# Performance work log

Hardware: AMD Instinct MI355X
Metric: run time of the kernel (lower is better)

## Reference

```python
import jax, jax.numpy as jnp
import numpy as np

OUTPUT_DIM = 1024
D_K = 1024  # Lt feature dim
D_Q = 1024  # rnn_ht feature dim
SCALE = 1.0 / np.sqrt(64.0)  # hardcoded 64**0.5 in original, NOT sqrt(output_dim)


def setup_inputs() -> dict:
    key = jax.random.key(0)
    k1, k2, k3, k4 = jax.random.split(key, 4)
    B, Sq, Sk = 8, 2048, 2048
    Lt = jax.random.normal(k1, (B, Sk, D_K), dtype=jnp.float32)
    rnn_ht = jax.random.normal(k2, (B, Sq, D_Q), dtype=jnp.float32)
    # 'uniform' keras initializer: U(-0.05, 0.05)
    kernel = jax.random.uniform(k3, (2, D_K, OUTPUT_DIM), dtype=jnp.float32, minval=-0.05, maxval=0.05)
    W = jax.random.uniform(k4, (D_Q, OUTPUT_DIM), dtype=jnp.float32, minval=-0.05, maxval=0.05)
    return {"Lt": Lt, "rnn_ht": rnn_ht, "kernel": kernel, "W": W}


def reference(Lt, rnn_ht, kernel, W):
    WQ = jnp.einsum('bsd,de->bse', rnn_ht, W)          # [B, Sq, E]
    WK = jnp.einsum('bsd,de->bse', Lt, kernel[0])      # [B, Sk, E]
    WV = jnp.einsum('bsd,de->bse', Lt, kernel[1])      # [B, Sk, E]
    QK = jnp.einsum('bqe,bke->bqk', WQ, WK) * SCALE    # [B, Sq, Sk]
    weights = jax.nn.softmax(QK, axis=-1)
    context_vector = jnp.einsum('bqk,bke->bqe', weights, WV)  # [B, Sq, E]
    return (context_vector, weights)
```

## Files before the change

### kernel.cpp

```cpp
#include <hip/hip_runtime.h>


typedef __bf16 bf16x8 __attribute__((ext_vector_type(8)));
typedef __bf16 bf16x4 __attribute__((ext_vector_type(4)));
typedef float  f32x4  __attribute__((ext_vector_type(4)));

__device__ __forceinline__ void gload_lds16(const void* g, void* l) {
  __builtin_amdgcn_global_load_lds(
      (__attribute__((address_space(1))) void*)(g),
      (__attribute__((address_space(3))) void*)(uintptr_t)(l),
      16, 0, 0);
}

__device__ __forceinline__ void ldfrag4(bf16x8 (&f)[4], const __bf16* reg_,
                                        int rbase, int fm, int gq) {
#pragma unroll
  for (int i = 0; i < 4; ++i) {
    const int r = rbase + i * 16 + fm;
    f[i] = *(const bf16x8*)(reg_ + r * 32 + ((gq ^ ((r >> 1) & 3)) << 3));
  }
}

__device__ __forceinline__ void stage16(const __bf16* src, __bf16* dst,
                                        size_t rowstride, int wave, int lane) {
#pragma unroll
  for (int i = 0; i < 2; ++i) {
    const int chunk = wave * 2 + i;
    const int row = chunk * 16 + (lane >> 2);
    const int gg = (lane & 3) ^ ((row >> 1) & 3);
    gload_lds16(src + (size_t)row * rowstride + (gg << 3), dst + chunk * 512);
  }
}

template <int MH>
__device__ __forceinline__ void mfma16(f32x4 (&acc)[8][4], const bf16x8 (&a)[4],
                                       const bf16x8 (&b)[4]) {
#pragma unroll
  for (int mi = 0; mi < 4; ++mi)
#pragma unroll
    for (int nj = 0; nj < 4; ++nj)
      acc[MH * 4 + mi][nj] = __builtin_amdgcn_mfma_f32_16x16x32_bf16(
          a[mi], b[nj], acc[MH * 4 + mi][nj], 0, 0, 0);
}

#define PHASE_MID()                       \
  __builtin_amdgcn_sched_barrier(0);      \
  __builtin_amdgcn_s_barrier();           \
  __builtin_amdgcn_s_setprio(1)

#define PHASE_END()                       \
  __builtin_amdgcn_s_setprio(0);          \
  __builtin_amdgcn_sched_barrier(0);      \
  __builtin_amdgcn_s_barrier()

template <bool OUTBF16>
__device__ __forceinline__ void tile_gemm(
    const __bf16* __restrict__ Aa, const __bf16* __restrict__ Ba,
    void* __restrict__ Cp, size_t cbase, int N, int K, float scale,
    __bf16* lds, int wave, int lane, int wm, int wn, int fm, int gq) {
  __bf16* const As_ = lds;
  __bf16* const Bs_ = lds + 32768;
#define AREG(p, h) (As_ + (p) * 16384 + (h) * 8192)
#define BREG(p, h) (Bs_ + (p) * 16384 + (h) * 8192)

  f32x4 acc[8][4] = {};
  bf16x8 a[4], b[4];

  stage16(Ba + 0,  BREG(0, 0), K, wave, lane);
  stage16(Aa + 0,  AREG(0, 0), K, wave, lane);
  stage16(Ba + 32, BREG(0, 1), K, wave, lane);
  stage16(Aa + 32, AREG(0, 1), K, wave, lane);
  asm volatile("s_waitcnt vmcnt(4)" ::: "memory");
  stage16(Ba + 64, BREG(1, 0), K, wave, lane);
  stage16(Aa + 64, AREG(1, 0), K, wave, lane);
  stage16(Ba + 96, BREG(1, 1), K, wave, lane);
  asm volatile("s_waitcnt vmcnt(6)" ::: "memory");
  __builtin_amdgcn_s_barrier();

  const int niter = K >> 7;
  for (int it = 0; it < niter; ++it) {
    const int kt = it << 7;
    const bool s2 = (kt + 128) < K;

    ldfrag4(a, AREG(0, 0), wm, fm, gq);
    ldfrag4(b, BREG(0, 0), wn, fm, gq);
    stage16(Aa + kt + 96, AREG(1, 1), K, wave, lane);
    PHASE_MID();
    mfma16<0>(acc, a, b);
    PHASE_END();

    ldfrag4(a, AREG(0, 0), wm + 64, fm, gq);
    if (s2) stage16(Ba + kt + 128, BREG(0, 0), K, wave, lane);
    PHASE_MID();
    mfma16<1>(acc, a, b);
    PHASE_END();

    ldfrag4(a, AREG(0, 1), wm, fm, gq);
    ldfrag4(b, BREG(0, 1), wn, fm, gq);
    if (s2) stage16(Aa + kt + 128, AREG(0, 0), K, wave, lane);
    PHASE_MID();
    mfma16<0>(acc, a, b);
    PHASE_END();

    ldfrag4(a, AREG(0, 1), wm + 64, fm, gq);
    if (s2) stage16(Ba + kt + 160, BREG(0, 1), K, wave, lane);
    PHASE_MID();
    mfma16<1>(acc, a, b);
    __builtin_amdgcn_s_setprio(0);
    __builtin_amdgcn_sched_barrier(0);
    if (s2) { asm volatile("s_waitcnt vmcnt(6)" ::: "memory"); }
    else    { asm volatile("s_waitcnt vmcnt(0)" ::: "memory"); }
    __builtin_amdgcn_s_barrier();

    ldfrag4(a, AREG(1, 0), wm, fm, gq);
    ldfrag4(b, BREG(1, 0), wn, fm, gq);
    if (s2) stage16(Aa + kt + 160, AREG(0, 1), K, wave, lane);
    PHASE_MID();
    mfma16<0>(acc, a, b);
    PHASE_END();

    ldfrag4(a, AREG(1, 0), wm + 64, fm, gq);
    if (s2) stage16(Ba + kt + 192, BREG(1, 0), K, wave, lane);
    PHASE_MID();
    mfma16<1>(acc, a, b);
    PHASE_END();

    ldfrag4(a, AREG(1, 1), wm, fm, gq);
    ldfrag4(b, BREG(1, 1), wn, fm, gq);
    if (s2) stage16(Aa + kt + 192, AREG(1, 0), K, wave, lane);
    PHASE_MID();
    mfma16<0>(acc, a, b);
    PHASE_END();

    ldfrag4(a, AREG(1, 1), wm + 64, fm, gq);
    if (s2) stage16(Ba + kt + 224, BREG(1, 1), K, wave, lane);
    PHASE_MID();
    mfma16<1>(acc, a, b);
    __builtin_amdgcn_s_setprio(0);
    __builtin_amdgcn_sched_barrier(0);
    if (s2) { asm volatile("s_waitcnt vmcnt(6)" ::: "memory"); }
    __builtin_amdgcn_s_barrier();
  }

  const int col   = lane & 15;
  const int rquad = (lane >> 4) * 4;
#pragma unroll
  for (int mi = 0; mi < 8; ++mi) {
#pragma unroll
    for (int r = 0; r < 4; ++r) {
      const size_t roff = (size_t)(wm + mi * 16 + rquad + r) * (size_t)N;
#pragma unroll
      for (int nj = 0; nj < 4; ++nj) {
        const size_t cidx = cbase + roff + wn + nj * 16 + col;
        if constexpr (OUTBF16) {
          ((__bf16*)Cp)[cidx] = (__bf16)acc[mi][nj][r];
        } else {
          ((float*)Cp)[cidx] = acc[mi][nj][r] * scale;
        }
      }
    }
  }
#undef AREG
#undef BREG
}

__global__ __launch_bounds__(512, 2)
void proj_all(const __bf16* __restrict__ rnnb, const __bf16* __restrict__ Ltb,
              const __bf16* __restrict__ Wt, const __bf16* __restrict__ k0t,
              const __bf16* __restrict__ k1t, __bf16* __restrict__ WQ,
              __bf16* __restrict__ WK, __bf16* __restrict__ WVt) {
  __shared__ __bf16 lds[65536];
  const int tid = threadIdx.x, wave = tid >> 6, lane = tid & 63;
  const int wm = (wave >> 2) * 128, wn = (wave & 3) * 64;
  const int fm = lane & 15, gq = lane >> 4;
  const int d = blockIdx.x, x = d & 7, s = d >> 3;

  {
    const int bx = s & 3, by = x * 8 + (s >> 2);
    const size_t ao = (size_t)by * 256 * 1024;
    const size_t bo = (size_t)bx * 256 * 1024;
    const size_t cb = (size_t)by * 256 * 1024 + (size_t)bx * 256;
    tile_gemm<true>(rnnb + ao, Wt + bo, WQ, cb, 1024, 1024, 1.0f,
                    lds, wave, lane, wm, wn, fm, gq);
    tile_gemm<true>(Ltb + ao, k0t + bo, WK, cb, 1024, 1024, 1.0f,
                    lds, wave, lane, wm, wn, fm, gq);
  }
  {
    const int by = s >> 3, bx = s & 7;
    tile_gemm<true>(k1t + (size_t)by * 256 * 1024,
                    Ltb + (size_t)x * 2048 * 1024 + (size_t)bx * 256 * 1024,
                    WVt,
                    (size_t)x * 1024 * 2048 + (size_t)by * 256 * 2048 +
                        (size_t)bx * 256,
                    2048, 1024, 1.0f, lds, wave, lane, wm, wn, fm, gq);
  }
}

__global__ __launch_bounds__(512, 2)
void qk2(const __bf16* __restrict__ WQ, const __bf16* __restrict__ WK,
         float* __restrict__ wts) {
  __shared__ __bf16 lds[65536];
  const int tid = threadIdx.x, wave = tid >> 6, lane = tid & 63;
  const int wm = (wave >> 2) * 128, wn = (wave & 3) * 64;
  const int fm = lane & 15, gq = lane >> 4;
  const int d = blockIdx.x, x = d & 7, s = d >> 3;
  const int by = s >> 3, bx = s & 7;

  const __bf16* Qb = WQ + (size_t)x * 2048 * 1024;
  const __bf16* Kb = WK + (size_t)x * 2048 * 1024 + (size_t)bx * 256 * 1024;
  const size_t cb0 = (size_t)x * 2048 * 2048 + (size_t)bx * 256;

  tile_gemm<false>(Qb + (size_t)by * 256 * 1024, Kb, wts,
                   cb0 + (size_t)by * 256 * 2048, 2048, 1024, 0.125f,
                   lds, wave, lane, wm, wn, fm, gq);
  tile_gemm<false>(Qb + (size_t)(by + 4) * 256 * 1024, Kb, wts,
                   cb0 + (size_t)(by + 4) * 256 * 2048, 2048, 1024, 0.125f,
                   lds, wave, lane, wm, wn, fm, gq);
}

__global__ __launch_bounds__(512, 2)
void pv1(const __bf16* __restrict__ Pb, const __bf16* __restrict__ WVt,
         float* __restrict__ ctx) {
  __shared__ __bf16 lds[65536];
  const int tid = threadIdx.x, wave = tid >> 6, lane = tid & 63;
  const int wm = (wave >> 2) * 128, wn = (wave & 3) * 64;
  const int fm = lane & 15, gq = lane >> 4;
  const int d = blockIdx.x, x = d & 7, s = d >> 3;
  const int by = s >> 2, bx = s & 3;

  tile_gemm<false>(Pb + (size_t)x * 2048 * 2048 + (size_t)by * 256 * 2048,
                   WVt + (size_t)x * 1024 * 2048 + (size_t)bx * 256 * 2048,
                   ctx,
                   (size_t)x * 2048 * 1024 + (size_t)by * 256 * 1024 +
                       (size_t)bx * 256,
                   1024, 2048, 1.0f, lds, wave, lane, wm, wn, fm, gq);
}

__global__ __launch_bounds__(256)
void cvt_transpose(const float* __restrict__ s0, const float* __restrict__ s1,
                   const float* __restrict__ s2, __bf16* __restrict__ d0,
                   __bf16* __restrict__ d1, __bf16* __restrict__ d2) {
  const float* s = blockIdx.z == 0 ? s0 : (blockIdx.z == 1 ? s1 : s2);
  __bf16* d      = blockIdx.z == 0 ? d0 : (blockIdx.z == 1 ? d1 : d2);
  __shared__ float tile[32][33];
  const int x  = blockIdx.x * 32 + threadIdx.x;
  const int y0 = blockIdx.y * 32;
  for (int j = threadIdx.y; j < 32; j += 8)
    tile[j][threadIdx.x] = s[(size_t)(y0 + j) * 1024 + x];
  __syncthreads();
  const int x2 = y0 + threadIdx.x;
  const int y2 = blockIdx.x * 32;
  for (int j = threadIdx.y; j < 32; j += 8)
    d[(size_t)(y2 + j) * 1024 + x2] = (__bf16)tile[threadIdx.x][j];
}

__global__ __launch_bounds__(256)
void cvt_bf16(const float* __restrict__ s0, __bf16* __restrict__ d0,
              const float* __restrict__ s1, __bf16* __restrict__ d1) {
  const float* s = blockIdx.z ? s1 : s0;
  __bf16* d      = blockIdx.z ? d1 : d0;
  const size_t i = ((size_t)blockIdx.x * 256 + threadIdx.x) * 4;
  float4 f = *(const float4*)(s + i);
  bf16x4 h = {(__bf16)f.x, (__bf16)f.y, (__bf16)f.z, (__bf16)f.w};
  *(bf16x4*)(d + i) = h;
}

__global__ __launch_bounds__(256)
void softmax_rows(float* __restrict__ Wt, __bf16* __restrict__ Pb) {
  const int t = threadIdx.x;
  float* p = Wt + (size_t)blockIdx.x * 2048;
  float4 a = ((float4*)p)[t];
  float4 b = ((float4*)p)[t + 256];

  float m = fmaxf(fmaxf(fmaxf(a.x, a.y), fmaxf(a.z, a.w)),
                  fmaxf(fmaxf(b.x, b.y), fmaxf(b.z, b.w)));
#pragma unroll
  for (int off = 32; off > 0; off >>= 1) m = fmaxf(m, __shfl_xor(m, off));
  __shared__ float red[8];
  if ((t & 63) == 0) red[t >> 6] = m;
  __syncthreads();
  m = fmaxf(fmaxf(red[0], red[1]), fmaxf(red[2], red[3]));

  a.x = __expf(a.x - m); a.y = __expf(a.y - m);
  a.z = __expf(a.z - m); a.w = __expf(a.w - m);
  b.x = __expf(b.x - m); b.y = __expf(b.y - m);
  b.z = __expf(b.z - m); b.w = __expf(b.w - m);
  float s = a.x + a.y + a.z + a.w + b.x + b.y + b.z + b.w;
#pragma unroll
  for (int off = 32; off > 0; off >>= 1) s += __shfl_xor(s, off);
  if ((t & 63) == 0) red[4 + (t >> 6)] = s;
  __syncthreads();
  s = red[4] + red[5] + red[6] + red[7];

  const float inv = 1.0f / s;
  a.x *= inv; a.y *= inv; a.z *= inv; a.w *= inv;
  b.x *= inv; b.y *= inv; b.z *= inv; b.w *= inv;
  ((float4*)p)[t] = a;
  ((float4*)p)[t + 256] = b;

  __bf16* pb = Pb + (size_t)blockIdx.x * 2048;
  bf16x4 ha = {(__bf16)a.x, (__bf16)a.y, (__bf16)a.z, (__bf16)a.w};
  bf16x4 hb = {(__bf16)b.x, (__bf16)b.y, (__bf16)b.z, (__bf16)b.w};
  *(bf16x4*)(pb + (size_t)t * 4) = ha;
  *(bf16x4*)(pb + (size_t)(t + 256) * 4) = hb;
}

extern "C" void kernel_launch(void* const* d_in, const int* in_sizes, int n_in,
                              void* d_out, int out_size, void* d_ws,
                              size_t ws_size, hipStream_t stream) {
  const float* Lt  = (const float*)d_in[0];
  const float* rnn = (const float*)d_in[1];
  const float* ker = (const float*)d_in[2];
  const float* W   = (const float*)d_in[3];

  float* ctx = (float*)d_out;
  float* wts = ctx + (size_t)16777216;

  __bf16* ws   = (__bf16*)d_ws;
  __bf16* Wt   = ws;
  __bf16* k0t  = Wt + (1u << 20);
  __bf16* k1t  = k0t + (1u << 20);
  __bf16* WQ   = k1t + (1u << 20);
  __bf16* WK   = WQ + (16u << 20);
  __bf16* WVt  = WK + (16u << 20);
  __bf16* Ltb  = WVt + (16u << 20);
  __bf16* rnnb = Ltb + (16u << 20);
  __bf16* Pb = Ltb;

  cvt_transpose<<<dim3(32, 32, 3), dim3(32, 8), 0, stream>>>(
      W, ker, ker + (1u << 20), Wt, k0t, k1t);

  cvt_bf16<<<dim3(16384, 1, 2), 256, 0, stream>>>(Lt, Ltb, rnn, rnnb);

  proj_all<<<256, 512, 0, stream>>>(rnnb, Ltb, Wt, k0t, k1t, WQ, WK, WVt);

  qk2<<<256, 512, 0, stream>>>(WQ, WK, wts);

  softmax_rows<<<16384, 256, 0, stream>>>(wts, Pb);

  pv1<<<256, 512, 0, stream>>>(Pb, WVt, ctx);
}
```

Measured before the change: 555.9 us.

## Fuse partial softmax into QK GEMM epilogue with bf16 logits and finalize pass

The QK GEMM epilogue now computes per-tile row maxima and partial exp sums, writes max-shifted logits as bf16, and stores the (max, sum) partials in a side buffer that reuses the transposed-weight workspace. A light finalize kernel combines the eight partials per row, then writes the fp32 weights and the bf16 probabilities. This replaces the fp32 read-modify-write of the full 2048x2048 score matrix with a bf16 intermediate, cutting global traffic between the GEMM and the softmax. In exchange, the logits are rounded to bf16 before exponentiation, which loses precision in the weights output, and the epilogue adds extra LDS reductions and barriers.

```diff
diff --git a/kernel.cpp b/kernel.cpp
--- a/kernel.cpp
+++ b/kernel.cpp
@@ -53,11 +53,12 @@
   __builtin_amdgcn_sched_barrier(0);      \
   __builtin_amdgcn_s_barrier()
 
-template <bool OUTBF16>
+template <int EPI>
 __device__ __forceinline__ void tile_gemm(
     const __bf16* __restrict__ Aa, const __bf16* __restrict__ Ba,
     void* __restrict__ Cp, size_t cbase, int N, int K, float scale,
-    __bf16* lds, int wave, int lane, int wm, int wn, int fm, int gq) {
+    __bf16* lds, int wave, int lane, int wm, int wn, int fm, int gq,
+    float* side, int sidebase) {
   __bf16* const As_ = lds;
   __bf16* const Bs_ = lds + 32768;
 #define AREG(p, h) (As_ + (p) * 16384 + (h) * 8192)
@@ -144,21 +145,78 @@
 
   const int col   = lane & 15;
   const int rquad = (lane >> 4) * 4;
-#pragma unroll
-  for (int mi = 0; mi < 8; ++mi) {
-#pragma unroll
-    for (int r = 0; r < 4; ++r) {
-      const size_t roff = (size_t)(wm + mi * 16 + rquad + r) * (size_t)N;
-#pragma unroll
-      for (int nj = 0; nj < 4; ++nj) {
-        const size_t cidx = cbase + roff + wn + nj * 16 + col;
-        if constexpr (OUTBF16) {
-          ((__bf16*)Cp)[cidx] = (__bf16)acc[mi][nj][r];
-        } else {
-          ((float*)Cp)[cidx] = acc[mi][nj][r] * scale;
+
+  if constexpr (EPI != 2) {
+#pragma unroll
+    for (int mi = 0; mi < 8; ++mi) {
+#pragma unroll
+      for (int r = 0; r < 4; ++r) {
+        const size_t roff = (size_t)(wm + mi * 16 + rquad + r) * (size_t)N;
+#pragma unroll
+        for (int nj = 0; nj < 4; ++nj) {
+          const size_t cidx = cbase + roff + wn + nj * 16 + col;
+          if constexpr (EPI == 1) {
+            ((__bf16*)Cp)[cidx] = (__bf16)acc[mi][nj][r];
+          } else {
+            ((float*)Cp)[cidx] = acc[mi][nj][r] * scale;
+          }
         }
       }
     }
+  } else {
+    const int tid = (wave << 6) | lane;
+    float* red  = (float*)lds;
+    float* mrow = red + 1024;
+#pragma unroll
+    for (int mi = 0; mi < 8; ++mi)
+#pragma unroll
+      for (int nj = 0; nj < 4; ++nj) acc[mi][nj] = acc[mi][nj] * scale;
+#pragma unroll
+    for (int mi = 0; mi < 8; ++mi) {
+#pragma unroll
+      for (int r = 0; r < 4; ++r) {
+        float vm = fmaxf(fmaxf(acc[mi][0][r], acc[mi][1][r]),
+                         fmaxf(acc[mi][2][r], acc[mi][3][r]));
+#pragma unroll
+        for (int off = 8; off > 0; off >>= 1)
+          vm = fmaxf(vm, __shfl_xor(vm, off));
+        if ((lane & 15) == 0)
+          red[(wave & 3) * 256 + wm + mi * 16 + rquad + r] = vm;
+      }
+    }
+    __syncthreads();
+    if (tid < 256)
+      mrow[tid] = fmaxf(fmaxf(red[tid], red[256 + tid]),
+                        fmaxf(red[512 + tid], red[768 + tid]));
+    __syncthreads();
+#pragma unroll
+    for (int mi = 0; mi < 8; ++mi) {
+#pragma unroll
+      for (int r = 0; r < 4; ++r) {
+        const int rloc = wm + mi * 16 + rquad + r;
+        const float m = mrow[rloc];
+        const size_t roff = (size_t)rloc * (size_t)N;
+        float ss = 0.f;
+#pragma unroll
+        for (int nj = 0; nj < 4; ++nj) {
+          const __bf16 hb = (__bf16)(acc[mi][nj][r] - m);
+          ((__bf16*)Cp)[cbase + roff + wn + nj * 16 + col] = hb;
+          ss += __expf((float)hb);
+        }
+#pragma unroll
+        for (int off = 8; off > 0; off >>= 1) ss += __shfl_xor(ss, off);
+        if ((lane & 15) == 0) red[(wave & 3) * 256 + rloc] = ss;
+      }
+    }
+    __syncthreads();
+    if (tid < 256) {
+      const float s =
+          red[tid] + red[256 + tid] + red[512 + tid] + red[768 + tid];
+      const size_t si = (size_t)(sidebase + tid * 8) * 2;
+      side[si]     = mrow[tid];
+      side[si + 1] = s;
+    }
+    __syncthreads();
   }
 #undef AREG
 #undef BREG
@@ -180,25 +238,26 @@
     const size_t ao = (size_t)by * 256 * 1024;
     const size_t bo = (size_t)bx * 256 * 1024;
     const size_t cb = (size_t)by * 256 * 1024 + (size_t)bx * 256;
-    tile_gemm<true>(rnnb + ao, Wt + bo, WQ, cb, 1024, 1024, 1.0f,
-                    lds, wave, lane, wm, wn, fm, gq);
-    tile_gemm<true>(Ltb + ao, k0t + bo, WK, cb, 1024, 1024, 1.0f,
-                    lds, wave, lane, wm, wn, fm, gq);
+    tile_gemm<1>(rnnb + ao, Wt + bo, WQ, cb, 1024, 1024, 1.0f,
+                 lds, wave, lane, wm, wn, fm, gq, nullptr, 0);
+    tile_gemm<1>(Ltb + ao, k0t + bo, WK, cb, 1024, 1024, 1.0f,
+                 lds, wave, lane, wm, wn, fm, gq, nullptr, 0);
   }
   {
     const int by = s >> 3, bx = s & 7;
-    tile_gemm<true>(k1t + (size_t)by * 256 * 1024,
-                    Ltb + (size_t)x * 2048 * 1024 + (size_t)bx * 256 * 1024,
-                    WVt,
-                    (size_t)x * 1024 * 2048 + (size_t)by * 256 * 2048 +
-                        (size_t)bx * 256,
-                    2048, 1024, 1.0f, lds, wave, lane, wm, wn, fm, gq);
+    tile_gemm<1>(k1t + (size_t)by * 256 * 1024,
+                 Ltb + (size_t)x * 2048 * 1024 + (size_t)bx * 256 * 1024,
+                 WVt,
+                 (size_t)x * 1024 * 2048 + (size_t)by * 256 * 2048 +
+                     (size_t)bx * 256,
+                 2048, 1024, 1.0f, lds, wave, lane, wm, wn, fm, gq,
+                 nullptr, 0);
   }
 }
 
 __global__ __launch_bounds__(512, 2)
-void qk2(const __bf16* __restrict__ WQ, const __bf16* __restrict__ WK,
-         float* __restrict__ wts) {
+void qk_sm(const __bf16* __restrict__ WQ, const __bf16* __restrict__ WK,
+           __bf16* __restrict__ Pb, float* __restrict__ side) {
   __shared__ __bf16 lds[65536];
   const int tid = threadIdx.x, wave = tid >> 6, lane = tid & 63;
   const int wm = (wave >> 2) * 128, wn = (wave & 3) * 64;
@@ -210,12 +269,52 @@
   const __bf16* Kb = WK + (size_t)x * 2048 * 1024 + (size_t)bx * 256 * 1024;
   const size_t cb0 = (size_t)x * 2048 * 2048 + (size_t)bx * 256;
 
-  tile_gemm<false>(Qb + (size_t)by * 256 * 1024, Kb, wts,
-                   cb0 + (size_t)by * 256 * 2048, 2048, 1024, 0.125f,
-                   lds, wave, lane, wm, wn, fm, gq);
-  tile_gemm<false>(Qb + (size_t)(by + 4) * 256 * 1024, Kb, wts,
-                   cb0 + (size_t)(by + 4) * 256 * 2048, 2048, 1024, 0.125f,
-                   lds, wave, lane, wm, wn, fm, gq);
+  tile_gemm<2>(Qb + (size_t)by * 256 * 1024, Kb, Pb,
+               cb0 + (size_t)by * 256 * 2048, 2048, 1024, 0.125f,
+               lds, wave, lane, wm, wn, fm, gq,
+               side, (x * 2048 + by * 256) * 8 + bx);
+  tile_gemm<2>(Qb + (size_t)(by + 4) * 256 * 1024, Kb, Pb,
+               cb0 + (size_t)(by + 4) * 256 * 2048, 2048, 1024, 0.125f,
+               lds, wave, lane, wm, wn, fm, gq,
+               side, (x * 2048 + (by + 4) * 256) * 8 + bx);
+}
+
+__global__ __launch_bounds__(256)
+void sm_finalize(const float* __restrict__ side, __bf16* __restrict__ Pb,
+                 float* __restrict__ wts) {
+  const size_t row = blockIdx.x;
+  const int t = threadIdx.x;
+  __shared__ float mt[8], st[8], fac[8];
+  if (t < 8) {
+    mt[t] = side[(row * 8 + t) * 2];
+    st[t] = side[(row * 8 + t) * 2 + 1];
+  }
+  __syncthreads();
+  if (t < 8) {
+    float mf = mt[0];
+#pragma unroll
+    for (int i = 1; i < 8; ++i) mf = fmaxf(mf, mt[i]);
+    float sf = 0.f;
+#pragma unroll
+    for (int i = 0; i < 8; ++i) sf += st[i] * __expf(mt[i] - mf);
+    fac[t] = __expf(mt[t] - mf) / sf;
+  }
+  __syncthreads();
+  __bf16* pb = Pb + row * 2048 + t * 8;
+  float*  w  = wts + row * 2048 + t * 8;
+  bf16x8 v = *(const bf16x8*)pb;
+  const float f = fac[t >> 5];
+  float wv[8];
+#pragma unroll
+  for (int i = 0; i < 8; ++i) wv[i] = __expf((float)v[i]) * f;
+  float4 w0 = {wv[0], wv[1], wv[2], wv[3]};
+  float4 w1 = {wv[4], wv[5], wv[6], wv[7]};
+  ((float4*)w)[0] = w0;
+  ((float4*)w)[1] = w1;
+  bf16x8 pv;
+#pragma unroll
+  for (int i = 0; i < 8; ++i) pv[i] = (__bf16)wv[i];
+  *(bf16x8*)pb = pv;
 }
 
 __global__ __launch_bounds__(512, 2)
@@ -228,12 +327,13 @@
   const int d = blockIdx.x, x = d & 7, s = d >> 3;
   const int by = s >> 2, bx = s & 3;
 
-  tile_gemm<false>(Pb + (size_t)x * 2048 * 2048 + (size_t)by * 256 * 2048,
-                   WVt + (size_t)x * 1024 * 2048 + (size_t)bx * 256 * 2048,
-                   ctx,
-                   (size_t)x * 2048 * 1024 + (size_t)by * 256 * 1024 +
-                       (size_t)bx * 256,
-                   1024, 2048, 1.0f, lds, wave, lane, wm, wn, fm, gq);
+  tile_gemm<0>(Pb + (size_t)x * 2048 * 2048 + (size_t)by * 256 * 2048,
+               WVt + (size_t)x * 1024 * 2048 + (size_t)bx * 256 * 2048,
+               ctx,
+               (size_t)x * 2048 * 1024 + (size_t)by * 256 * 1024 +
+                   (size_t)bx * 256,
+               1024, 2048, 1.0f, lds, wave, lane, wm, wn, fm, gq,
+               nullptr, 0);
 }
 
 __global__ __launch_bounds__(256)
@@ -265,46 +365,6 @@
   *(bf16x4*)(d + i) = h;
 }
 
-__global__ __launch_bounds__(256)
-void softmax_rows(float* __restrict__ Wt, __bf16* __restrict__ Pb) {
-  const int t = threadIdx.x;
-  float* p = Wt + (size_t)blockIdx.x * 2048;
-  float4 a = ((float4*)p)[t];
-  float4 b = ((float4*)p)[t + 256];
-
-  float m = fmaxf(fmaxf(fmaxf(a.x, a.y), fmaxf(a.z, a.w)),
-                  fmaxf(fmaxf(b.x, b.y), fmaxf(b.z, b.w)));
-#pragma unroll
-  for (int off = 32; off > 0; off >>= 1) m = fmaxf(m, __shfl_xor(m, off));
-  __shared__ float red[8];
-  if ((t & 63) == 0) red[t >> 6] = m;
-  __syncthreads();
-  m = fmaxf(fmaxf(red[0], red[1]), fmaxf(red[2], red[3]));
-
-  a.x = __expf(a.x - m); a.y = __expf(a.y - m);
-  a.z = __expf(a.z - m); a.w = __expf(a.w - m);
-  b.x = __expf(b.x - m); b.y = __expf(b.y - m);
-  b.z = __expf(b.z - m); b.w = __expf(b.w - m);
-  float s = a.x + a.y + a.z + a.w + b.x + b.y + b.z + b.w;
-#pragma unroll
-  for (int off = 32; off > 0; off >>= 1) s += __shfl_xor(s, off);
-  if ((t & 63) == 0) red[4 + (t >> 6)] = s;
-  __syncthreads();
-  s = red[4] + red[5] + red[6] + red[7];
-
-  const float inv = 1.0f / s;
-  a.x *= inv; a.y *= inv; a.z *= inv; a.w *= inv;
-  b.x *= inv; b.y *= inv; b.z *= inv; b.w *= inv;
-  ((float4*)p)[t] = a;
-  ((float4*)p)[t + 256] = b;
-
-  __bf16* pb = Pb + (size_t)blockIdx.x * 2048;
-  bf16x4 ha = {(__bf16)a.x, (__bf16)a.y, (__bf16)a.z, (__bf16)a.w};
-  bf16x4 hb = {(__bf16)b.x, (__bf16)b.y, (__bf16)b.z, (__bf16)b.w};
-  *(bf16x4*)(pb + (size_t)t * 4) = ha;
-  *(bf16x4*)(pb + (size_t)(t + 256) * 4) = hb;
-}
-
 extern "C" void kernel_launch(void* const* d_in, const int* in_sizes, int n_in,
                               void* d_out, int out_size, void* d_ws,
                               size_t ws_size, hipStream_t stream) {
@@ -326,6 +386,7 @@
   __bf16* Ltb  = WVt + (16u << 20);
   __bf16* rnnb = Ltb + (16u << 20);
   __bf16* Pb = Ltb;
+  float* side = (float*)Wt;
 
   cvt_transpose<<<dim3(32, 32, 3), dim3(32, 8), 0, stream>>>(
       W, ker, ker + (1u << 20), Wt, k0t, k1t);
@@ -334,9 +395,9 @@
 
   proj_all<<<256, 512, 0, stream>>>(rnnb, Ltb, Wt, k0t, k1t, WQ, WK, WVt);
 
-  qk2<<<256, 512, 0, stream>>>(WQ, WK, wts);
-
-  softmax_rows<<<16384, 256, 0, stream>>>(wts, Pb);
+  qk_sm<<<256, 512, 0, stream>>>(WQ, WK, Pb, side);
+
+  sm_finalize<<<16384, 256, 0, stream>>>(side, Pb, wts);
 
   pv1<<<256, 512, 0, stream>>>(Pb, WVt, ctx);
 }
```

Result: slower. 598.7 us (+7.7%).
